# Kernel optimization log

Measured on AMD Instinct MI355X. Metric: run time of the kernel, lower is better.

## Reference

```python
import jax, jax.numpy as jnp
import numpy as np

N_NODES = 100000
N_EDGES = 1600000


def _degree_norms(src, dst, n):
    ones = jnp.ones(src.shape[0], dtype=jnp.float32)
    deg_out = jax.ops.segment_sum(ones, src, num_segments=n)
    deg_in = jax.ops.segment_sum(ones, dst, num_segments=n)
    src_norm = jax.lax.rsqrt(jnp.maximum(deg_out, 1.0))
    dst_norm = jax.lax.rsqrt(jnp.maximum(deg_in, 1.0))
    return src_norm, dst_norm


def _graph_conv(x, W, b, src, dst, src_norm, dst_norm, n):
    # DGL GraphConv, norm='both': D_dst^{-1/2} A D_src^{-1/2} X W + b
    # Apply W first (same math, smaller messages).
    h = x @ W                                  # [N, out]
    m = (h * src_norm[:, None])[src]           # [E, out] gather
    agg = jax.ops.segment_sum(m, dst, num_segments=n)  # [N, out] scatter-add
    return agg * dst_norm[:, None] + b


def setup_inputs() -> dict:
    key = jax.random.key(0)
    ks = jax.random.split(key, 10)
    inp = {
        "x": jax.random.normal(ks[0], (N_NODES, 128), dtype=jnp.float32),
        "src": jax.random.randint(ks[1], (N_EDGES,), 0, N_NODES, dtype=jnp.int32),
        "dst": jax.random.randint(ks[2], (N_EDGES,), 0, N_NODES, dtype=jnp.int32),
        "W1": jax.random.normal(ks[3], (128, 64), dtype=jnp.float32) * 0.08,
        "b1": jnp.zeros((64,), dtype=jnp.float32),
        "W2": jax.random.normal(ks[4], (64, 64), dtype=jnp.float32) * 0.12,
        "b2": jnp.zeros((64,), dtype=jnp.float32),
        "W3": jax.random.normal(ks[5], (64, 64), dtype=jnp.float32) * 0.12,
        "b3": jnp.zeros((64,), dtype=jnp.float32),
        "W4": jax.random.normal(ks[6], (64, 64), dtype=jnp.float32) * 0.12,
        "b4": jnp.zeros((64,), dtype=jnp.float32),
        "Wres": jax.random.normal(ks[7], (128, 64), dtype=jnp.float32) * 0.08,
        "bres": jnp.zeros((64,), dtype=jnp.float32),
        "Wop": jax.random.normal(ks[8], (64, 16), dtype=jnp.float32) * 0.12,
        "bop": jnp.zeros((16,), dtype=jnp.float32),
    }
    return inp


def reference(x, src, dst, W1, b1, W2, b2, W3, b3, W4, b4, Wres, bres, Wop, bop):
    n = x.shape[0]
    src_norm, dst_norm = _degree_norms(src, dst, n)
    res = x @ Wres + bres
    out = jax.nn.relu(_graph_conv(x, W1, b1, src, dst, src_norm, dst_norm, n))
    out = jax.nn.relu(_graph_conv(out, W2, b2, src, dst, src_norm, dst_norm, n))
    out = jax.nn.relu(_graph_conv(out, W3, b3, src, dst, src_norm, dst_norm, n))
    out = _graph_conv(out, W4, b4, src, dst, src_norm, dst_norm, n)
    out = jax.nn.relu(out + res)
    return out @ Wop + bop
```

## Files before the change

kernel.cpp:

```cpp
#include <hip/hip_runtime.h>
#include <cstdint>
#include <cstddef>


#define SLOTS 64
#define BCAP 5120
#define ACHUNK 4096

typedef __attribute__((ext_vector_type(8))) short bf16x8;
typedef __attribute__((ext_vector_type(4))) float f32x4;

__device__ __forceinline__ unsigned short f2bf(float f) {
  union { float f; unsigned u; } v; v.f = f;
  unsigned r = (v.u + 0x7fffu + ((v.u >> 16) & 1u)) >> 16;
  return (unsigned short)r;
}
__device__ __forceinline__ void bf2x2(unsigned u, float* lo, float* hi) {
  union { unsigned x; float f; } a, b;
  a.x = u << 16; b.x = u & 0xFFFF0000u;
  *lo = a.f; *hi = b.f;
}
__device__ __forceinline__ bf16x8 cvt8(float4 f0, float4 f1) {
  bf16x8 v;
  v[0] = (short)f2bf(f0.x); v[1] = (short)f2bf(f0.y);
  v[2] = (short)f2bf(f0.z); v[3] = (short)f2bf(f0.w);
  v[4] = (short)f2bf(f1.x); v[5] = (short)f2bf(f1.y);
  v[6] = (short)f2bf(f1.z); v[7] = (short)f2bf(f1.w);
  return v;
}

#define UNPACK_ADD(u, A)                         \
  { float f0_, f1_, f2_, f3_;                    \
    bf2x2((u).x, &f0_, &f1_);                    \
    bf2x2((u).y, &f2_, &f3_);                    \
    A[0] += f0_; A[1] += f1_; A[2] += f2_; A[3] += f3_; }

__global__ void prep_kernel(const float* __restrict__ W1, const float* __restrict__ W2,
                            const float* __restrict__ W3, const float* __restrict__ W4,
                            const float* __restrict__ Wres,
                            unsigned short* __restrict__ WT,
                            int* __restrict__ gcur_d, int* __restrict__ gcur_s, int nbuck) {
  int i = blockIdx.x * blockDim.x + threadIdx.x;
  if (i < nbuck) { gcur_d[i] = 0; gcur_s[i] = 0; }
  if (i < 8192) {
    int c = i >> 7, k = i & 127;
    WT[i] = f2bf(W1[k * 64 + c]);
  } else if (i < 12288) {
    int j = i - 8192; int c = j >> 6, k = j & 63;
    WT[i] = f2bf(W2[k * 64 + c]);
  } else if (i < 16384) {
    int j = i - 12288; int c = j >> 6, k = j & 63;
    WT[i] = f2bf(W3[k * 64 + c]);
  } else if (i < 20480) {
    int j = i - 16384; int c = j >> 6, k = j & 63;
    WT[i] = f2bf(W4[k * 64 + c]);
  } else if (i < 28672) {
    int j = i - 20480; int c = j >> 7, k = j & 127;
    WT[i] = f2bf(Wres[k * 64 + c]);
  }
}

__global__ __launch_bounds__(256) void bucket_kernel(
    const int* __restrict__ src, const int* __restrict__ dst,
    int* __restrict__ gcur_d, int* __restrict__ gcur_s,
    unsigned* __restrict__ dbuck, unsigned char* __restrict__ sbuck,
    int E, int nbuck) {
  __shared__ int s_src[ACHUNK];
  __shared__ int s_dst[ACHUNK];
  __shared__ int run_d[512];
  __shared__ int run_s[512];
  const int t = threadIdx.x;
  const int base = blockIdx.x * ACHUNK;
  int cnt = E - base;
  if (cnt > ACHUNK) cnt = ACHUNK;

  for (int i = t; i < cnt; i += 256) {
    s_src[i] = src[base + i];
    s_dst[i] = dst[base + i];
  }
  for (int i = t; i < nbuck; i += 256) { run_d[i] = 0; run_s[i] = 0; }
  __syncthreads();
  for (int i = t; i < cnt; i += 256) {
    atomicAdd(&run_d[s_dst[i] >> 8], 1);
    atomicAdd(&run_s[s_src[i] >> 8], 1);
  }
  __syncthreads();
  {
    const int iters = (nbuck + 255) >> 8;
    for (int it = 0; it < iters; ++it) {
      int i = it * 256 + t;
      int hd = 0, hs = 0;
      if (i < nbuck) { hd = run_d[i]; hs = run_s[i]; }
      __syncthreads();
      if (i < nbuck) {
        run_d[i] = hd ? atomicAdd(&gcur_d[i], hd) : 0;
        run_s[i] = hs ? atomicAdd(&gcur_s[i], hs) : 0;
      }
      __syncthreads();
    }
  }
  for (int i = t; i < cnt; i += 256) {
    int d = s_dst[i], s = s_src[i];
    int bd = d >> 8;
    int pd = atomicAdd(&run_d[bd], 1);
    if (pd < BCAP) dbuck[(size_t)bd * BCAP + pd] = ((unsigned)(d & 255) << 24) | (unsigned)s;
    int bs = s >> 8;
    int ps = atomicAdd(&run_s[bs], 1);
    if (ps < BCAP) sbuck[(size_t)bs * BCAP + ps] = (unsigned char)(s & 255);
  }
}

__global__ __launch_bounds__(256) void csr_kernel(
    const unsigned* __restrict__ dbuck, const int* __restrict__ gcur_d,
    int* __restrict__ col, int* __restrict__ cnt_arr,
    float* __restrict__ dnorm, int N) {
  __shared__ int cur[256];
  const int b = blockIdx.x;
  const int t = threadIdx.x;
  const int node0 = b << 8;
  cur[t] = 0;
  __syncthreads();
  int cnt = gcur_d[b];
  if (cnt > BCAP) cnt = BCAP;
  const unsigned* p = dbuck + (size_t)b * BCAP;
  for (int i = t; i < cnt; i += 256) {
    unsigned e = p[i];
    int nl = e >> 24;
    int s = (int)(e & 0x00FFFFFFu);
    int pos = atomicAdd(&cur[nl], 1);
    if (pos < SLOTS) col[(size_t)(node0 + nl) * SLOTS + pos] = s;
  }
  __syncthreads();
  int node = node0 + t;
  if (node < N) {
    int c = cur[t];
    cnt_arr[node] = c;
    float d = (float)(c < 1 ? 1 : c);
    dnorm[node] = rsqrtf(d);
  }
}

__global__ __launch_bounds__(256) void degout_kernel(
    const unsigned char* __restrict__ sbuck, const int* __restrict__ gcur_s,
    float* __restrict__ snorm, int N) {
  __shared__ int cur[256];
  const int b = blockIdx.x;
  const int t = threadIdx.x;
  cur[t] = 0;
  __syncthreads();
  int cnt = gcur_s[b];
  if (cnt > BCAP) cnt = BCAP;
  const unsigned char* p = sbuck + (size_t)b * BCAP;
  for (int i = t; i < cnt; i += 256) atomicAdd(&cur[p[i]], 1);
  __syncthreads();
  int node = (b << 8) + t;
  if (node < N) {
    int c = cur[t];
    snorm[node] = rsqrtf((float)(c < 1 ? 1 : c));
  }
}

__global__ __launch_bounds__(256) void gemm1_mfma_kernel(
    const float* __restrict__ X, const unsigned short* __restrict__ W1T,
    const unsigned short* __restrict__ WresT, const float* __restrict__ bres,
    const float* __restrict__ norm,
    unsigned short* __restrict__ Hout, unsigned short* __restrict__ Rout, int n) {
  __shared__ float ol[64][68];
  const int t = threadIdx.x;
  const int l = t & 63;
  const int w = t >> 6;
  const int node0 = blockIdx.x * 64;
  const int row = l & 15, kg = l >> 4;

  int arow = node0 + w * 16 + row;
  if (arow > n - 1) arow = n - 1;
  const float* ap = X + (size_t)arow * 128 + kg * 8;
  bf16x8 a[4];
#pragma unroll
  for (int kh = 0; kh < 4; kh++) {
    float4 f0 = *(const float4*)(ap + kh * 32);
    float4 f1 = *(const float4*)(ap + kh * 32 + 4);
    a[kh] = cvt8(f0, f1);
  }

  f32x4 acc[4], acc2[4];
#pragma unroll
  for (int ct = 0; ct < 4; ct++) {
    acc[ct] = (f32x4){0.f, 0.f, 0.f, 0.f};
    acc2[ct] = (f32x4){0.f, 0.f, 0.f, 0.f};
  }

#pragma unroll
  for (int kh = 0; kh < 4; kh++) {
#pragma unroll
    for (int ct = 0; ct < 4; ct++) {
      const unsigned short* wb1 = W1T + (size_t)(ct * 16 + row) * 128 + kh * 32 + kg * 8;
      const unsigned short* wbr = WresT + (size_t)(ct * 16 + row) * 128 + kh * 32 + kg * 8;
      bf16x8 b1 = *(const bf16x8*)(wb1);
      bf16x8 br = *(const bf16x8*)(wbr);
      acc[ct] = __builtin_amdgcn_mfma_f32_16x16x32_bf16(a[kh], b1, acc[ct], 0, 0, 0);
      acc2[ct] = __builtin_amdgcn_mfma_f32_16x16x32_bf16(a[kh], br, acc2[ct], 0, 0, 0);
    }
  }

#pragma unroll
  for (int ct = 0; ct < 4; ct++)
#pragma unroll
    for (int i = 0; i < 4; i++)
      ol[w * 16 + kg * 4 + i][ct * 16 + row] = acc[ct][i];
  __syncthreads();
  {
    int r2 = t >> 2, cg = (t & 3) * 16;
    int node = node0 + r2;
    if (node < n) {
      float s = norm[node];
      unsigned short o[16];
#pragma unroll
      for (int i = 0; i < 16; i++) o[i] = f2bf(ol[r2][cg + i] * s);
      *(uint4*)&Hout[(size_t)node * 64 + cg] = *(const uint4*)&o[0];
      *(uint4*)&Hout[(size_t)node * 64 + cg + 8] = *(const uint4*)&o[8];
    }
  }
  __syncthreads();
#pragma unroll
  for (int ct = 0; ct < 4; ct++)
#pragma unroll
    for (int i = 0; i < 4; i++)
      ol[w * 16 + kg * 4 + i][ct * 16 + row] = acc2[ct][i];
  __syncthreads();
  {
    int r2 = t >> 2, cg = (t & 3) * 16;
    int node = node0 + r2;
    if (node < n) {
      unsigned short o[16];
#pragma unroll
      for (int i = 0; i < 16; i++) o[i] = f2bf(ol[r2][cg + i] + bres[cg + i]);
      *(uint4*)&Rout[(size_t)node * 64 + cg] = *(const uint4*)&o[0];
      *(uint4*)&Rout[(size_t)node * 64 + cg + 8] = *(const uint4*)&o[8];
    }
  }
}

__global__ __launch_bounds__(256) void gemm_mfma_kernel(
    const unsigned short* __restrict__ X, const unsigned short* __restrict__ WT,
    const float* __restrict__ norm, unsigned short* __restrict__ out, int n) {
  __shared__ float ol[64][68];
  const int t = threadIdx.x;
  const int l = t & 63;
  const int w = t >> 6;
  const int node0 = blockIdx.x * 64;
  const int row = l & 15, kg = l >> 4;

  int arow = node0 + w * 16 + row;
  if (arow > n - 1) arow = n - 1;
  const unsigned short* ab = X + (size_t)arow * 64 + kg * 8;
  bf16x8 a0 = *(const bf16x8*)(ab);
  bf16x8 a1 = *(const bf16x8*)(ab + 32);

  f32x4 acc[4];
#pragma unroll
  for (int ct = 0; ct < 4; ct++) acc[ct] = (f32x4){0.f, 0.f, 0.f, 0.f};

#pragma unroll
  for (int ct = 0; ct < 4; ct++) {
    const unsigned short* wb = WT + (size_t)(ct * 16 + row) * 64 + kg * 8;
    bf16x8 b0 = *(const bf16x8*)(wb);
    bf16x8 b1 = *(const bf16x8*)(wb + 32);
    acc[ct] = __builtin_amdgcn_mfma_f32_16x16x32_bf16(a0, b0, acc[ct], 0, 0, 0);
    acc[ct] = __builtin_amdgcn_mfma_f32_16x16x32_bf16(a1, b1, acc[ct], 0, 0, 0);
  }

#pragma unroll
  for (int ct = 0; ct < 4; ct++)
#pragma unroll
    for (int i = 0; i < 4; i++)
      ol[w * 16 + kg * 4 + i][ct * 16 + row] = acc[ct][i];
  __syncthreads();

  {
    int r2 = t >> 2, cg = (t & 3) * 16;
    int node = node0 + r2;
    if (node < n) {
      float s = norm[node];
      unsigned short o[16];
#pragma unroll
      for (int i = 0; i < 16; i++) o[i] = f2bf(ol[r2][cg + i] * s);
      *(uint4*)&out[(size_t)node * 64 + cg] = *(const uint4*)&o[0];
      *(uint4*)&out[(size_t)node * 64 + cg + 8] = *(const uint4*)&o[8];
    }
  }
}

template <int RELU>
__global__ __launch_bounds__(256) void agg_kernel(
    const unsigned short* __restrict__ H, const int* __restrict__ cnt_arr,
    const int* __restrict__ col, const float* __restrict__ dnorm,
    const float* __restrict__ bias, unsigned short* __restrict__ O,
    int n) {
  const int lane = threadIdx.x & 63;
  const int sub = lane >> 4;
  const int fl  = lane & 15;
  const int wave = (blockIdx.x * blockDim.x + threadIdx.x) >> 6;
  const int nwaves = (gridDim.x * blockDim.x) >> 6;
  const uint2* __restrict__ H2 = (const uint2*)H;
  const float4 bb = ((const float4*)bias)[fl];

  for (int v0 = wave * 2; v0 < n; v0 += nwaves * 2) {
    const int v1 = v0 + 1;
    int cnt0 = cnt_arr[v0];
    int cnt1 = (v1 < n) ? cnt_arr[v1] : 0;
    if (cnt0 > SLOTS) cnt0 = SLOTS;
    if (cnt1 > SLOTS) cnt1 = SLOTS;
    const size_t base0 = (size_t)v0 * SLOTS;
    const size_t base1 = (size_t)v1 * SLOTS;
    int cv0 = (lane < cnt0) ? col[base0 + lane] : 0;
    int cv1 = (lane < cnt1) ? col[base1 + lane] : 0;
    float a0[4] = {0.f, 0.f, 0.f, 0.f};
    float b0[4] = {0.f, 0.f, 0.f, 0.f};
    float a1[4] = {0.f, 0.f, 0.f, 0.f};
    float b1[4] = {0.f, 0.f, 0.f, 0.f};
    const int cmax = cnt0 > cnt1 ? cnt0 : cnt1;
    for (int j = 0; j < cmax; j += 8) {
      const int e0 = j + sub;
      const int e1 = j + 4 + sub;
      int c00 = __shfl(cv0, e0);
      int c01 = __shfl(cv0, e1);
      int c10 = __shfl(cv1, e0);
      int c11 = __shfl(cv1, e1);
      if (e0 < cnt0) { uint2 u = H2[(size_t)c00 * 16 + fl]; UNPACK_ADD(u, a0) }
      if (e0 < cnt1) { uint2 u = H2[(size_t)c10 * 16 + fl]; UNPACK_ADD(u, a1) }
      if (e1 < cnt0) { uint2 u = H2[(size_t)c01 * 16 + fl]; UNPACK_ADD(u, b0) }
      if (e1 < cnt1) { uint2 u = H2[(size_t)c11 * 16 + fl]; UNPACK_ADD(u, b1) }
    }
    float r0[4], r1[4];
#pragma unroll
    for (int i = 0; i < 4; i++) {
      float s0 = a0[i] + b0[i];
      s0 += __shfl_xor(s0, 16);
      s0 += __shfl_xor(s0, 32);
      r0[i] = s0;
      float s1 = a1[i] + b1[i];
      s1 += __shfl_xor(s1, 16);
      s1 += __shfl_xor(s1, 32);
      r1[i] = s1;
    }
    if (sub == 0) {
      float d = dnorm[v0];
      float q0 = r0[0] * d + bb.x;
      float q1 = r0[1] * d + bb.y;
      float q2 = r0[2] * d + bb.z;
      float q3 = r0[3] * d + bb.w;
      if (RELU) {
        q0 = fmaxf(q0, 0.f); q1 = fmaxf(q1, 0.f);
        q2 = fmaxf(q2, 0.f); q3 = fmaxf(q3, 0.f);
      }
      ushort4 o;
      o.x = f2bf(q0); o.y = f2bf(q1); o.z = f2bf(q2); o.w = f2bf(q3);
      *(ushort4*)&O[base0 + 4 * fl] = o;
    } else if (sub == 1 && v1 < n) {
      float d = dnorm[v1];
      float q0 = r1[0] * d + bb.x;
      float q1 = r1[1] * d + bb.y;
      float q2 = r1[2] * d + bb.z;
      float q3 = r1[3] * d + bb.w;
      if (RELU) {
        q0 = fmaxf(q0, 0.f); q1 = fmaxf(q1, 0.f);
        q2 = fmaxf(q2, 0.f); q3 = fmaxf(q3, 0.f);
      }
      ushort4 o;
      o.x = f2bf(q0); o.y = f2bf(q1); o.z = f2bf(q2); o.w = f2bf(q3);
      *(ushort4*)&O[base1 + 4 * fl] = o;
    }
  }
}

__global__ __launch_bounds__(256) void final_kernel(
    const unsigned short* __restrict__ O4, const unsigned short* __restrict__ R,
    const float* __restrict__ Wop, const float* __restrict__ bop,
    float* __restrict__ out, int n) {
  __shared__ float t_lds[64][68];
  __shared__ float wop_lds[64][16];
  const int t = threadIdx.x;
  const int node0 = blockIdx.x * 64;
  const int srow = t >> 2;
  const int scol = (t & 3) * 16;

  ((float4*)&wop_lds[0][0])[t] = ((const float4*)Wop)[t];

  {
    int gi = node0 + srow;
    float f[16];
    if (gi < n) {
      const unsigned short* po = O4 + (size_t)gi * 64 + scol;
      const unsigned short* pr = R + (size_t)gi * 64 + scol;
      uint4 uo0 = *(const uint4*)(po + 0);
      uint4 uo1 = *(const uint4*)(po + 8);
      uint4 ur0 = *(const uint4*)(pr + 0);
      uint4 ur1 = *(const uint4*)(pr + 8);
      float o0, o1, rr0, rr1;
#define ADDRELU2(UO, UR, idx)                         \
      bf2x2(UO, &o0, &o1); bf2x2(UR, &rr0, &rr1);     \
      f[idx] = fmaxf(o0 + rr0, 0.f);                  \
      f[idx + 1] = fmaxf(o1 + rr1, 0.f);
      ADDRELU2(uo0.x, ur0.x, 0)  ADDRELU2(uo0.y, ur0.y, 2)
      ADDRELU2(uo0.z, ur0.z, 4)  ADDRELU2(uo0.w, ur0.w, 6)
      ADDRELU2(uo1.x, ur1.x, 8)  ADDRELU2(uo1.y, ur1.y, 10)
      ADDRELU2(uo1.z, ur1.z, 12) ADDRELU2(uo1.w, ur1.w, 14)
#undef ADDRELU2
    } else {
#pragma unroll
      for (int j = 0; j < 16; j++) f[j] = 0.f;
    }
#pragma unroll
    for (int j = 0; j < 16; j += 4)
      *(float4*)&t_lds[srow][scol + j] = make_float4(f[j], f[j+1], f[j+2], f[j+3]);
  }
  __syncthreads();

  {
    int nn = t >> 2;
    int fg = t & 3;
    float4 a = ((const float4*)bop)[fg];
#pragma unroll 16
    for (int k = 0; k < 64; k++) {
      float tv = t_lds[nn][k];
      float4 w = *(const float4*)&wop_lds[k][fg * 4];
      a.x = fmaf(tv, w.x, a.x);
      a.y = fmaf(tv, w.y, a.y);
      a.z = fmaf(tv, w.z, a.z);
      a.w = fmaf(tv, w.w, a.w);
    }
    int node = node0 + nn;
    if (node < n) *(float4*)&out[(size_t)node * 16 + fg * 4] = a;
  }
}

extern "C" void kernel_launch(void* const* d_in, const int* in_sizes, int n_in,
                              void* d_out, int out_size, void* d_ws, size_t ws_size,
                              hipStream_t stream) {
  const float* x    = (const float*)d_in[0];
  const int*   src  = (const int*)d_in[1];
  const int*   dst  = (const int*)d_in[2];
  const float* W1   = (const float*)d_in[3];
  const float* b1   = (const float*)d_in[4];
  const float* W2   = (const float*)d_in[5];
  const float* b2   = (const float*)d_in[6];
  const float* W3   = (const float*)d_in[7];
  const float* b3   = (const float*)d_in[8];
  const float* W4   = (const float*)d_in[9];
  const float* b4   = (const float*)d_in[10];
  const float* Wres = (const float*)d_in[11];
  const float* bres = (const float*)d_in[12];
  const float* Wop  = (const float*)d_in[13];
  const float* bop  = (const float*)d_in[14];
  float* out = (float*)d_out;

  const int N = in_sizes[0] / 128;
  const int E = in_sizes[1];
  const int nbuck = (N + 255) >> 8;

  char* p = (char*)d_ws;
  auto alloc = [&](size_t b) {
    char* r = p;
    p += (b + 255) & ~(size_t)255;
    return r;
  };
  int*            gcur_d  = (int*)alloc((size_t)nbuck * 4);
  int*            gcur_s  = (int*)alloc((size_t)nbuck * 4);
  unsigned short* WT      = (unsigned short*)alloc(28672 * 2);
  unsigned*       dbuck   = (unsigned*)alloc((size_t)nbuck * BCAP * 4);
  unsigned char*  sbuck   = (unsigned char*)alloc((size_t)nbuck * BCAP);
  int*            col     = (int*)alloc((size_t)N * SLOTS * 4);
  int*            cnt_arr = (int*)alloc((size_t)N * 4);
  float*          snorm   = (float*)alloc((size_t)N * 4);
  float*          dnorm   = (float*)alloc((size_t)N * 4);
  unsigned short* Hbuf    = (unsigned short*)alloc((size_t)N * 64 * 2);
  unsigned short* Obuf    = (unsigned short*)alloc((size_t)N * 64 * 2);
  unsigned short* Rbuf    = (unsigned short*)alloc((size_t)N * 64 * 2);

  unsigned short* W1T   = WT;
  unsigned short* W2T   = WT + 8192;
  unsigned short* W3T   = WT + 12288;
  unsigned short* W4T   = WT + 16384;
  unsigned short* WresT = WT + 20480;

  prep_kernel<<<112, 256, 0, stream>>>(W1, W2, W3, W4, Wres, WT, gcur_d, gcur_s, nbuck);

  int ga = (E + ACHUNK - 1) / ACHUNK;
  bucket_kernel<<<ga, 256, 0, stream>>>(src, dst, gcur_d, gcur_s, dbuck, sbuck, E, nbuck);
  csr_kernel<<<nbuck, 256, 0, stream>>>(dbuck, gcur_d, col, cnt_arr, dnorm, N);
  degout_kernel<<<nbuck, 256, 0, stream>>>(sbuck, gcur_s, snorm, N);

  int gb = (N + 63) / 64;
  gemm1_mfma_kernel<<<gb, 256, 0, stream>>>(x, W1T, WresT, bres, snorm, Hbuf, Rbuf, N);
  agg_kernel<1><<<2048, 256, 0, stream>>>(Hbuf, cnt_arr, col, dnorm, b1, Obuf, N);
  gemm_mfma_kernel<<<gb, 256, 0, stream>>>(Obuf, W2T, snorm, Hbuf, N);
  agg_kernel<1><<<2048, 256, 0, stream>>>(Hbuf, cnt_arr, col, dnorm, b2, Obuf, N);
  gemm_mfma_kernel<<<gb, 256, 0, stream>>>(Obuf, W3T, snorm, Hbuf, N);
  agg_kernel<1><<<2048, 256, 0, stream>>>(Hbuf, cnt_arr, col, dnorm, b3, Obuf, N);
  gemm_mfma_kernel<<<gb, 256, 0, stream>>>(Obuf, W4T, snorm, Hbuf, N);
  agg_kernel<0><<<2048, 256, 0, stream>>>(Hbuf, cnt_arr, col, dnorm, b4, Obuf, N);
  final_kernel<<<gb, 256, 0, stream>>>(Obuf, Rbuf, Wop, bop, out, N);
}
```

Measured before the change: 306.1 us.

## Fuse CSR and out-degree kernels, drop LDS epilogue in GEMMs, halve bucket chunk

Merges the CSR build and out-degree count into one kernel, removing a launch and a pass over the bucket metadata. The GEMM kernels now write results straight from MFMA accumulators with 2-byte scalar stores instead of staging through shared memory, which removes LDS traffic and barriers but gives less coalesced global writes. The bucket chunk size is halved so the bucketing kernel launches more blocks, which raises parallelism at the cost of more global atomics on the bucket cursors.

```diff
diff --git a/kernel.cpp b/kernel.cpp
--- a/kernel.cpp
+++ b/kernel.cpp
@@ -5,7 +5,7 @@
 
 #define SLOTS 64
 #define BCAP 5120
-#define ACHUNK 4096
+#define ACHUNK 2048
 
 typedef __attribute__((ext_vector_type(8))) short bf16x8;
 typedef __attribute__((ext_vector_type(4))) float f32x4;
@@ -78,7 +78,7 @@
     s_src[i] = src[base + i];
     s_dst[i] = dst[base + i];
   }
-  for (int i = t; i < nbuck; i += 256) { run_d[i] = 0; run_s[i] = 0; }
+  for (int i = t; i < 512; i += 256) { run_d[i] = 0; run_s[i] = 0; }
   __syncthreads();
   for (int i = t; i < cnt; i += 256) {
     atomicAdd(&run_d[s_dst[i] >> 8], 1);
@@ -110,53 +110,41 @@
   }
 }
 
-__global__ __launch_bounds__(256) void csr_kernel(
+__global__ __launch_bounds__(256) void csrdeg_kernel(
     const unsigned* __restrict__ dbuck, const int* __restrict__ gcur_d,
+    const unsigned char* __restrict__ sbuck, const int* __restrict__ gcur_s,
     int* __restrict__ col, int* __restrict__ cnt_arr,
-    float* __restrict__ dnorm, int N) {
+    float* __restrict__ dnorm, float* __restrict__ snorm, int N) {
   __shared__ int cur[256];
+  __shared__ int curs[256];
   const int b = blockIdx.x;
   const int t = threadIdx.x;
   const int node0 = b << 8;
   cur[t] = 0;
+  curs[t] = 0;
   __syncthreads();
-  int cnt = gcur_d[b];
-  if (cnt > BCAP) cnt = BCAP;
+  int cntd = gcur_d[b];
+  if (cntd > BCAP) cntd = BCAP;
   const unsigned* p = dbuck + (size_t)b * BCAP;
-  for (int i = t; i < cnt; i += 256) {
+  for (int i = t; i < cntd; i += 256) {
     unsigned e = p[i];
     int nl = e >> 24;
     int s = (int)(e & 0x00FFFFFFu);
     int pos = atomicAdd(&cur[nl], 1);
     if (pos < SLOTS) col[(size_t)(node0 + nl) * SLOTS + pos] = s;
   }
+  int cnts = gcur_s[b];
+  if (cnts > BCAP) cnts = BCAP;
+  const unsigned char* ps = sbuck + (size_t)b * BCAP;
+  for (int i = t; i < cnts; i += 256) atomicAdd(&curs[ps[i]], 1);
   __syncthreads();
   int node = node0 + t;
   if (node < N) {
     int c = cur[t];
     cnt_arr[node] = c;
-    float d = (float)(c < 1 ? 1 : c);
-    dnorm[node] = rsqrtf(d);
-  }
-}
-
-__global__ __launch_bounds__(256) void degout_kernel(
-    const unsigned char* __restrict__ sbuck, const int* __restrict__ gcur_s,
-    float* __restrict__ snorm, int N) {
-  __shared__ int cur[256];
-  const int b = blockIdx.x;
-  const int t = threadIdx.x;
-  cur[t] = 0;
-  __syncthreads();
-  int cnt = gcur_s[b];
-  if (cnt > BCAP) cnt = BCAP;
-  const unsigned char* p = sbuck + (size_t)b * BCAP;
-  for (int i = t; i < cnt; i += 256) atomicAdd(&cur[p[i]], 1);
-  __syncthreads();
-  int node = (b << 8) + t;
-  if (node < N) {
-    int c = cur[t];
-    snorm[node] = rsqrtf((float)(c < 1 ? 1 : c));
+    dnorm[node] = rsqrtf((float)(c < 1 ? 1 : c));
+    int cs = curs[t];
+    snorm[node] = rsqrtf((float)(cs < 1 ? 1 : cs));
   }
 }
 
@@ -165,14 +153,13 @@
     const unsigned short* __restrict__ WresT, const float* __restrict__ bres,
     const float* __restrict__ norm,
     unsigned short* __restrict__ Hout, unsigned short* __restrict__ Rout, int n) {
-  __shared__ float ol[64][68];
   const int t = threadIdx.x;
   const int l = t & 63;
   const int w = t >> 6;
   const int node0 = blockIdx.x * 64;
-  const int row = l & 15, kg = l >> 4;
-
-  int arow = node0 + w * 16 + row;
+  const int cc16 = l & 15, kg = l >> 4;
+
+  int arow = node0 + w * 16 + cc16;
   if (arow > n - 1) arow = n - 1;
   const float* ap = X + (size_t)arow * 128 + kg * 8;
   bf16x8 a[4];
@@ -194,8 +181,8 @@
   for (int kh = 0; kh < 4; kh++) {
 #pragma unroll
     for (int ct = 0; ct < 4; ct++) {
-      const unsigned short* wb1 = W1T + (size_t)(ct * 16 + row) * 128 + kh * 32 + kg * 8;
-      const unsigned short* wbr = WresT + (size_t)(ct * 16 + row) * 128 + kh * 32 + kg * 8;
+      const unsigned short* wb1 = W1T + (size_t)(ct * 16 + cc16) * 128 + kh * 32 + kg * 8;
+      const unsigned short* wbr = WresT + (size_t)(ct * 16 + cc16) * 128 + kh * 32 + kg * 8;
       bf16x8 b1 = *(const bf16x8*)(wb1);
       bf16x8 br = *(const bf16x8*)(wbr);
       acc[ct] = __builtin_amdgcn_mfma_f32_16x16x32_bf16(a[kh], b1, acc[ct], 0, 0, 0);
@@ -203,40 +190,25 @@
     }
   }
 
-#pragma unroll
-  for (int ct = 0; ct < 4; ct++)
-#pragma unroll
-    for (int i = 0; i < 4; i++)
-      ol[w * 16 + kg * 4 + i][ct * 16 + row] = acc[ct][i];
-  __syncthreads();
-  {
-    int r2 = t >> 2, cg = (t & 3) * 16;
-    int node = node0 + r2;
-    if (node < n) {
-      float s = norm[node];
-      unsigned short o[16];
-#pragma unroll
-      for (int i = 0; i < 16; i++) o[i] = f2bf(ol[r2][cg + i] * s);
-      *(uint4*)&Hout[(size_t)node * 64 + cg] = *(const uint4*)&o[0];
-      *(uint4*)&Hout[(size_t)node * 64 + cg + 8] = *(const uint4*)&o[8];
-    }
-  }
-  __syncthreads();
-#pragma unroll
-  for (int ct = 0; ct < 4; ct++)
-#pragma unroll
-    for (int i = 0; i < 4; i++)
-      ol[w * 16 + kg * 4 + i][ct * 16 + row] = acc2[ct][i];
-  __syncthreads();
-  {
-    int r2 = t >> 2, cg = (t & 3) * 16;
-    int node = node0 + r2;
-    if (node < n) {
-      unsigned short o[16];
-#pragma unroll
-      for (int i = 0; i < 16; i++) o[i] = f2bf(ol[r2][cg + i] + bres[cg + i]);
-      *(uint4*)&Rout[(size_t)node * 64 + cg] = *(const uint4*)&o[0];
-      *(uint4*)&Rout[(size_t)node * 64 + cg + 8] = *(const uint4*)&o[8];
+  float sn[4];
+  int nd[4];
+  bool ok[4];
+#pragma unroll
+  for (int i = 0; i < 4; i++) {
+    nd[i] = node0 + w * 16 + kg * 4 + i;
+    ok[i] = nd[i] < n;
+    sn[i] = ok[i] ? norm[nd[i]] : 0.f;
+  }
+#pragma unroll
+  for (int ct = 0; ct < 4; ct++) {
+    const int c = ct * 16 + cc16;
+    const float bv = bres[c];
+#pragma unroll
+    for (int i = 0; i < 4; i++) {
+      if (ok[i]) {
+        Hout[(size_t)nd[i] * 64 + c] = f2bf(acc[ct][i] * sn[i]);
+        Rout[(size_t)nd[i] * 64 + c] = f2bf(acc2[ct][i] + bv);
+      }
     }
   }
 }
@@ -244,14 +216,13 @@
 __global__ __launch_bounds__(256) void gemm_mfma_kernel(
     const unsigned short* __restrict__ X, const unsigned short* __restrict__ WT,
     const float* __restrict__ norm, unsigned short* __restrict__ out, int n) {
-  __shared__ float ol[64][68];
   const int t = threadIdx.x;
   const int l = t & 63;
   const int w = t >> 6;
   const int node0 = blockIdx.x * 64;
-  const int row = l & 15, kg = l >> 4;
-
-  int arow = node0 + w * 16 + row;
+  const int cc16 = l & 15, kg = l >> 4;
+
+  int arow = node0 + w * 16 + cc16;
   if (arow > n - 1) arow = n - 1;
   const unsigned short* ab = X + (size_t)arow * 64 + kg * 8;
   bf16x8 a0 = *(const bf16x8*)(ab);
@@ -263,30 +234,28 @@
 
 #pragma unroll
   for (int ct = 0; ct < 4; ct++) {
-    const unsigned short* wb = WT + (size_t)(ct * 16 + row) * 64 + kg * 8;
+    const unsigned short* wb = WT + (size_t)(ct * 16 + cc16) * 64 + kg * 8;
     bf16x8 b0 = *(const bf16x8*)(wb);
     bf16x8 b1 = *(const bf16x8*)(wb + 32);
     acc[ct] = __builtin_amdgcn_mfma_f32_16x16x32_bf16(a0, b0, acc[ct], 0, 0, 0);
     acc[ct] = __builtin_amdgcn_mfma_f32_16x16x32_bf16(a1, b1, acc[ct], 0, 0, 0);
   }
 
-#pragma unroll
-  for (int ct = 0; ct < 4; ct++)
-#pragma unroll
-    for (int i = 0; i < 4; i++)
-      ol[w * 16 + kg * 4 + i][ct * 16 + row] = acc[ct][i];
-  __syncthreads();
-
-  {
-    int r2 = t >> 2, cg = (t & 3) * 16;
-    int node = node0 + r2;
-    if (node < n) {
-      float s = norm[node];
-      unsigned short o[16];
-#pragma unroll
-      for (int i = 0; i < 16; i++) o[i] = f2bf(ol[r2][cg + i] * s);
-      *(uint4*)&out[(size_t)node * 64 + cg] = *(const uint4*)&o[0];
-      *(uint4*)&out[(size_t)node * 64 + cg + 8] = *(const uint4*)&o[8];
+  float sn[4];
+  int nd[4];
+  bool ok[4];
+#pragma unroll
+  for (int i = 0; i < 4; i++) {
+    nd[i] = node0 + w * 16 + kg * 4 + i;
+    ok[i] = nd[i] < n;
+    sn[i] = ok[i] ? norm[nd[i]] : 0.f;
+  }
+#pragma unroll
+  for (int ct = 0; ct < 4; ct++) {
+    const int c = ct * 16 + cc16;
+#pragma unroll
+    for (int i = 0; i < 4; i++) {
+      if (ok[i]) out[(size_t)nd[i] * 64 + c] = f2bf(acc[ct][i] * sn[i]);
     }
   }
 }
@@ -488,8 +457,8 @@
 
   int ga = (E + ACHUNK - 1) / ACHUNK;
   bucket_kernel<<<ga, 256, 0, stream>>>(src, dst, gcur_d, gcur_s, dbuck, sbuck, E, nbuck);
-  csr_kernel<<<nbuck, 256, 0, stream>>>(dbuck, gcur_d, col, cnt_arr, dnorm, N);
-  degout_kernel<<<nbuck, 256, 0, stream>>>(sbuck, gcur_s, snorm, N);
+  csrdeg_kernel<<<nbuck, 256, 0, stream>>>(dbuck, gcur_d, sbuck, gcur_s,
+                                           col, cnt_arr, dnorm, snorm, N);
 
   int gb = (N + 63) / 64;
   gemm1_mfma_kernel<<<gb, 256, 0, stream>>>(x, W1T, WresT, bres, snorm, Hbuf, Rbuf, N);
```

After: 321.9 us. 1.05x slower.
